# Optimization experiments

Measured on AMD Instinct MI355X. Metric: run time of the kernel, lower is better.

Reference implementation:

```python
import jax, jax.numpy as jnp
import numpy as np

N, C, NS = 131072, 128, 16
BN_EPS = 1e-5


def setup_inputs() -> dict:
    key = jax.random.key(0)
    ks = jax.random.split(key, 8)
    p = jax.random.normal(ks[0], (N, 3), dtype=jnp.float32)
    u = jax.random.normal(ks[1], (N, C), dtype=jnp.float32)
    o = jnp.array([N], dtype=jnp.int32)  # batch offset (single cloud)
    idx = jax.random.randint(ks[2], (N, NS), 0, N, dtype=jnp.int32)  # precomputed KNN indices
    s = 1.0 / np.sqrt(C)
    W1 = jax.random.uniform(ks[3], (C, C), jnp.float32, -s, s)
    b1 = jax.random.uniform(ks[4], (C,), jnp.float32, -s, s)
    W2 = jax.random.uniform(ks[5], (C, C), jnp.float32, -s, s)
    b2 = jax.random.uniform(ks[6], (C,), jnp.float32, -s, s)
    gamma = jnp.ones((C,), jnp.float32)
    beta = jnp.zeros((C,), jnp.float32)
    return {"p": p, "u": u, "o": o, "idx": idx, "W1": W1, "b1": b1,
            "W2": W2, "b2": b2, "gamma": gamma, "beta": beta}


def reference(p, u, o, idx, W1, b1, W2, b2, gamma, beta):
    # pre_trans: Linear(d_in, d_in)
    u_pre = u @ W1 + b1                                  # [N, C]
    # queryandgroup (use_xyz=False): gather neighbor features by KNN idx
    u_n = u_pre[idx]                                     # [N, NS, C] irregular gather
    # local Laplacian: ReLU(neighbor - center), mean over neighborhood
    lap = jnp.maximum(u_n - u_pre[:, None, :], 0.0).mean(axis=1)  # [N, C]
    # varphi: Linear -> BatchNorm1d (training stats) -> ReLU
    h = lap @ W2 + b2                                    # [N, C]
    mean = h.mean(axis=0)
    var = ((h - mean) ** 2).mean(axis=0)  # biased var, as BN normalization uses
    h = (h - mean) * jax.lax.rsqrt(var + BN_EPS) * gamma + beta
    u_tt = jnp.maximum(h, 0.0)
    return (p, u_tt, o)
```

## Files before the change

kernel.cpp:

```cpp
#include <hip/hip_runtime.h>

#define N_PTS 131072
#define C_DIM 128
#define NS_K  16
#define BN_EPS 1e-5f

typedef unsigned short ushort_t;
typedef unsigned short u16x8 __attribute__((ext_vector_type(8)));
typedef __bf16 bf16x8 __attribute__((ext_vector_type(8)));
typedef float f32x4 __attribute__((ext_vector_type(4)));

__device__ __forceinline__ ushort_t f2b(float f) {
    unsigned int u = __float_as_uint(f);
    u += 0x7FFFu + ((u >> 16) & 1u);
    return (ushort_t)(u >> 16);
}
__device__ __forceinline__ float b2f(ushort_t h) {
    return __uint_as_float((unsigned int)h << 16);
}

__global__ __launch_bounds__(256) void prep_w_kernel(
    const float* __restrict__ W1, const float* __restrict__ W2,
    ushort_t* __restrict__ wT1, ushort_t* __restrict__ wT2)
{
    const int t = blockIdx.x * 256 + threadIdx.x;
    const int n = t & 127;
    const int k = t >> 7;
    wT1[n * 128 + k] = f2b(W1[k * 128 + n]);
    wT2[n * 128 + k] = f2b(W2[k * 128 + n]);
}

template <bool A_BF16, bool STATS>
__global__ __launch_bounds__(256) void gemm_mfma_kernel(
    const void* __restrict__ Aptr, const ushort_t* __restrict__ wT,
    const float* __restrict__ bias, ushort_t* __restrict__ out,
    float* __restrict__ gsum, float* __restrict__ gsq)
{
    __shared__ __align__(16) ushort_t a_sh[128 * 136];
    __shared__ __align__(16) ushort_t w_sh[128 * 136];
    __shared__ float s_sum[128];
    __shared__ float s_sq[128];

    const int tid  = threadIdx.x;
    const int lane = tid & 63;
    const int wv   = tid >> 6;
    const int m16  = lane & 15;
    const int q    = lane >> 4;
    const int base = blockIdx.x * 128;

    if (STATS && tid < 128) { s_sum[tid] = 0.f; s_sq[tid] = 0.f; }

    {
        const int row  = tid >> 1;
        const int half = (tid & 1) * 64;
        ushort_t* as = a_sh + row * 136 + half;
        if (A_BF16) {
            const ushort_t* ag = (const ushort_t*)Aptr + (size_t)(base + row) * 128 + half;
            #pragma unroll
            for (int j = 0; j < 8; j++)
                *(u16x8*)(as + j * 8) = *(const u16x8*)(ag + j * 8);
        } else {
            const float* ag = (const float*)Aptr + (size_t)(base + row) * 128 + half;
            #pragma unroll
            for (int j = 0; j < 8; j++) {
                f32x4 lo = *(const f32x4*)(ag + j * 8);
                f32x4 hi = *(const f32x4*)(ag + j * 8 + 4);
                u16x8 v;
                v[0] = f2b(lo[0]); v[1] = f2b(lo[1]); v[2] = f2b(lo[2]); v[3] = f2b(lo[3]);
                v[4] = f2b(hi[0]); v[5] = f2b(hi[1]); v[6] = f2b(hi[2]); v[7] = f2b(hi[3]);
                *(u16x8*)(as + j * 8) = v;
            }
        }
    }
    {
        const int n    = tid >> 1;
        const int half = (tid & 1) * 64;
        const ushort_t* wg = wT + (size_t)n * 128 + half;
        ushort_t* ws = w_sh + n * 136 + half;
        #pragma unroll
        for (int j = 0; j < 8; j++)
            *(u16x8*)(ws + j * 8) = *(const u16x8*)(wg + j * 8);
    }
    __syncthreads();

    f32x4 acc[2][8];
    #pragma unroll
    for (int i = 0; i < 2; i++)
        #pragma unroll
        for (int c = 0; c < 8; c++) acc[i][c] = (f32x4){0.f, 0.f, 0.f, 0.f};

    const ushort_t* ap0 = a_sh + ((wv * 2 + 0) * 16 + m16) * 136 + q * 8;
    const ushort_t* ap1 = a_sh + ((wv * 2 + 1) * 16 + m16) * 136 + q * 8;
    const ushort_t* wp  = w_sh + m16 * 136 + q * 8;

    #pragma unroll
    for (int k0 = 0; k0 < 128; k0 += 32) {
        bf16x8 a0 = __builtin_bit_cast(bf16x8, *(const u16x8*)(ap0 + k0));
        bf16x8 a1 = __builtin_bit_cast(bf16x8, *(const u16x8*)(ap1 + k0));
        #pragma unroll
        for (int c = 0; c < 8; c++) {
            bf16x8 b = __builtin_bit_cast(bf16x8, *(const u16x8*)(wp + c * (16 * 136) + k0));
            acc[0][c] = __builtin_amdgcn_mfma_f32_16x16x32_bf16(a0, b, acc[0][c], 0, 0, 0);
            acc[1][c] = __builtin_amdgcn_mfma_f32_16x16x32_bf16(a1, b, acc[1][c], 0, 0, 0);
        }
    }

    __syncthreads();

    float psum[8], psq[8];
    #pragma unroll
    for (int c = 0; c < 8; c++) { psum[c] = 0.f; psq[c] = 0.f; }

    #pragma unroll
    for (int c = 0; c < 8; c++) {
        const int col = c * 16 + m16;
        const float bv = bias[col];
        #pragma unroll
        for (int i = 0; i < 2; i++) {
            const int rb = (wv * 2 + i) * 16 + q * 4;
            #pragma unroll
            for (int r = 0; r < 4; r++) {
                const float v = acc[i][c][r] + bv;
                a_sh[(rb + r) * 136 + col] = f2b(v);
                if (STATS) { psum[c] += v; psq[c] += v * v; }
            }
        }
    }
    if (STATS) {
        #pragma unroll
        for (int c = 0; c < 8; c++) {
            atomicAdd(&s_sum[c * 16 + m16], psum[c]);
            atomicAdd(&s_sq[c * 16 + m16],  psq[c]);
        }
    }
    __syncthreads();

    {
        const int r0 = tid >> 4;
        const int c0 = (tid & 15) * 8;
        #pragma unroll
        for (int it = 0; it < 8; it++) {
            const int rl = r0 + it * 16;
            const u16x8 v = *(const u16x8*)(a_sh + rl * 136 + c0);
            *(u16x8*)(out + (size_t)(base + rl) * 128 + c0) = v;
        }
    }
    if (STATS && tid < 128) {
        atomicAdd(&gsum[tid], s_sum[tid]);
        atomicAdd(&gsq[tid],  s_sq[tid]);
    }
}

__global__ __launch_bounds__(256) void laplacian_kernel(
    const ushort_t* __restrict__ table, const int* __restrict__ idx,
    ushort_t* __restrict__ lap)
{
    __shared__ int s_idx[256];
    const int tid = threadIdx.x;
    s_idx[tid] = idx[blockIdx.x * 256 + tid];
    __syncthreads();

    const int p  = tid >> 4;
    const int c8 = (tid & 15) * 8;
    const size_t pt = (size_t)blockIdx.x * 16 + p;

    const u16x8 cv = *(const u16x8*)(table + pt * 128 + c8);
    float ctr[8];
    #pragma unroll
    for (int e = 0; e < 8; e++) ctr[e] = b2f(cv[e]);

    float acc[8];
    #pragma unroll
    for (int e = 0; e < 8; e++) acc[e] = 0.f;

    #pragma unroll
    for (int s = 0; s < NS_K; s++) {
        const int j = s_idx[p * 16 + s];
        const u16x8 nv = *(const u16x8*)(table + (size_t)j * 128 + c8);
        #pragma unroll
        for (int e = 0; e < 8; e++)
            acc[e] += fmaxf(b2f(nv[e]) - ctr[e], 0.f);
    }

    u16x8 o;
    #pragma unroll
    for (int e = 0; e < 8; e++) o[e] = f2b(acc[e] * (1.f / (float)NS_K));
    *(u16x8*)(lap + pt * 128 + c8) = o;
}

__global__ void bn_stats_kernel(const float* __restrict__ gsum,
                                const float* __restrict__ gsq,
                                const float* __restrict__ gamma,
                                const float* __restrict__ beta,
                                float* __restrict__ bnsc, float* __restrict__ bnsh)
{
    const int c = threadIdx.x;
    const float invN = 1.f / (float)N_PTS;
    const float mean = gsum[c] * invN;
    const float var  = gsq[c] * invN - mean * mean;
    const float sc   = rsqrtf(var + BN_EPS) * gamma[c];
    bnsc[c] = sc;
    bnsh[c] = fmaf(-mean, sc, beta[c]);
}

__global__ __launch_bounds__(256) void bn_relu_kernel(
    const ushort_t* __restrict__ h, const float* __restrict__ bnsc,
    const float* __restrict__ bnsh, float* __restrict__ out)
{
    const size_t i = (size_t)blockIdx.x * 256 + threadIdx.x;
    const int c8 = (threadIdx.x * 8) & 127;

    const u16x8 hv = *(const u16x8*)(h + i * 8);
    const f32x4 sc0 = *(const f32x4*)(bnsc + c8);
    const f32x4 sc1 = *(const f32x4*)(bnsc + c8 + 4);
    const f32x4 sh0 = *(const f32x4*)(bnsh + c8);
    const f32x4 sh1 = *(const f32x4*)(bnsh + c8 + 4);

    f32x4 o0, o1;
    #pragma unroll
    for (int e = 0; e < 4; e++) {
        o0[e] = fmaxf(fmaf(b2f(hv[e]),     sc0[e], sh0[e]), 0.f);
        o1[e] = fmaxf(fmaf(b2f(hv[4 + e]), sc1[e], sh1[e]), 0.f);
    }
    float* op = out + (size_t)3 * N_PTS + i * 8;
    *(f32x4*)(op)     = o0;
    *(f32x4*)(op + 4) = o1;
}

__global__ __launch_bounds__(256) void copy_p_kernel(
    const float* __restrict__ p, const int* __restrict__ o,
    float* __restrict__ out)
{
    const size_t i = (size_t)blockIdx.x * 256 + threadIdx.x;
    *(f32x4*)(out + i * 4) = *(const f32x4*)(p + i * 4);
    if (i == 0)
        out[(size_t)3 * N_PTS + (size_t)N_PTS * C_DIM] = (float)o[0];
}

extern "C" void kernel_launch(void* const* d_in, const int* in_sizes, int n_in,
                              void* d_out, int out_size, void* d_ws, size_t ws_size,
                              hipStream_t stream) {
    const float* p     = (const float*)d_in[0];
    const float* u     = (const float*)d_in[1];
    const int*   o     = (const int*)d_in[2];
    const int*   idx   = (const int*)d_in[3];
    const float* W1    = (const float*)d_in[4];
    const float* b1    = (const float*)d_in[5];
    const float* W2    = (const float*)d_in[6];
    const float* b2    = (const float*)d_in[7];
    const float* gamma = (const float*)d_in[8];
    const float* beta  = (const float*)d_in[9];
    float* out = (float*)d_out;

    char* ws = (char*)d_ws;
    const size_t buf_bytes = (size_t)N_PTS * C_DIM * sizeof(ushort_t);
    ushort_t* table = (ushort_t*)ws;
    ushort_t* lap   = (ushort_t*)(ws + buf_bytes);
    ushort_t* h     = (ushort_t*)(ws + 2 * buf_bytes);
    float*    stats = (float*)(ws + 3 * buf_bytes);
    float* gsum = stats;
    float* gsq  = stats + 128;
    float* bnsc = stats + 256;
    float* bnsh = stats + 384;
    ushort_t* wT1 = (ushort_t*)(stats + 512);
    ushort_t* wT2 = wT1 + 128 * 128;

    hipMemsetAsync(stats, 0, 256 * sizeof(float), stream);

    prep_w_kernel<<<64, 256, 0, stream>>>(W1, W2, wT1, wT2);
    gemm_mfma_kernel<false, false><<<N_PTS / 128, 256, 0, stream>>>(
        u, wT1, b1, table, nullptr, nullptr);
    laplacian_kernel<<<N_PTS / 16, 256, 0, stream>>>(table, idx, lap);
    gemm_mfma_kernel<true, true><<<N_PTS / 128, 256, 0, stream>>>(
        lap, wT2, b2, h, gsum, gsq);
    bn_stats_kernel<<<1, 128, 0, stream>>>(gsum, gsq, gamma, beta, bnsc, bnsh);
    bn_relu_kernel<<<(N_PTS * C_DIM / 8) / 256, 256, 0, stream>>>(
        h, bnsc, bnsh, out);
    copy_p_kernel<<<(3 * N_PTS / 4) / 256, 256, 0, stream>>>(p, o, out);
}
```

Measured before the change: 288.3 us.

## Fuse BN stats, BN+ReLU and p-copy into one kernel; read weights from global

Removes the memset by zeroing the stats in the weight-prep kernel. Merges the bn_stats, bn_relu and copy_p kernels into one launch that computes the BN scale and shift per block in shared memory. The GEMM kernels no longer stage the 128x128 weight tile in LDS; B fragments are read straight from global or L2. The GEMMs also get a 3-blocks-per-SM launch bound. This cuts launch count and LDS footprint, but adds repeated global weight reads inside the MFMA loop.

```diff
diff --git a/kernel.cpp b/kernel.cpp
--- a/kernel.cpp
+++ b/kernel.cpp
@@ -21,25 +21,26 @@
 
 __global__ __launch_bounds__(256) void prep_w_kernel(
     const float* __restrict__ W1, const float* __restrict__ W2,
-    ushort_t* __restrict__ wT1, ushort_t* __restrict__ wT2)
+    ushort_t* __restrict__ wT1, ushort_t* __restrict__ wT2,
+    float* __restrict__ stats)
 {
     const int t = blockIdx.x * 256 + threadIdx.x;
     const int n = t & 127;
     const int k = t >> 7;
     wT1[n * 128 + k] = f2b(W1[k * 128 + n]);
     wT2[n * 128 + k] = f2b(W2[k * 128 + n]);
+    if (blockIdx.x == 0) stats[threadIdx.x] = 0.f;
 }
 
 template <bool A_BF16, bool STATS>
-__global__ __launch_bounds__(256) void gemm_mfma_kernel(
+__global__ __launch_bounds__(256, 3) void gemm_mfma_kernel(
     const void* __restrict__ Aptr, const ushort_t* __restrict__ wT,
     const float* __restrict__ bias, ushort_t* __restrict__ out,
     float* __restrict__ gsum, float* __restrict__ gsq)
 {
     __shared__ __align__(16) ushort_t a_sh[128 * 136];
-    __shared__ __align__(16) ushort_t w_sh[128 * 136];
-    __shared__ float s_sum[128];
-    __shared__ float s_sq[128];
+    __shared__ float s_sum[STATS ? 128 : 1];
+    __shared__ float s_sq[STATS ? 128 : 1];
 
     const int tid  = threadIdx.x;
     const int lane = tid & 63;
@@ -72,15 +73,6 @@
             }
         }
     }
-    {
-        const int n    = tid >> 1;
-        const int half = (tid & 1) * 64;
-        const ushort_t* wg = wT + (size_t)n * 128 + half;
-        ushort_t* ws = w_sh + n * 136 + half;
-        #pragma unroll
-        for (int j = 0; j < 8; j++)
-            *(u16x8*)(ws + j * 8) = *(const u16x8*)(wg + j * 8);
-    }
     __syncthreads();
 
     f32x4 acc[2][8];
@@ -91,7 +83,7 @@
 
     const ushort_t* ap0 = a_sh + ((wv * 2 + 0) * 16 + m16) * 136 + q * 8;
     const ushort_t* ap1 = a_sh + ((wv * 2 + 1) * 16 + m16) * 136 + q * 8;
-    const ushort_t* wp  = w_sh + m16 * 136 + q * 8;
+    const ushort_t* wp  = wT + (size_t)m16 * 128 + q * 8;
 
     #pragma unroll
     for (int k0 = 0; k0 < 128; k0 += 32) {
@@ -99,7 +91,8 @@
         bf16x8 a1 = __builtin_bit_cast(bf16x8, *(const u16x8*)(ap1 + k0));
         #pragma unroll
         for (int c = 0; c < 8; c++) {
-            bf16x8 b = __builtin_bit_cast(bf16x8, *(const u16x8*)(wp + c * (16 * 136) + k0));
+            bf16x8 b = __builtin_bit_cast(bf16x8,
+                *(const u16x8*)(wp + c * (16 * 128) + k0));
             acc[0][c] = __builtin_amdgcn_mfma_f32_16x16x32_bf16(a0, b, acc[0][c], 0, 0, 0);
             acc[1][c] = __builtin_amdgcn_mfma_f32_16x16x32_bf16(a1, b, acc[1][c], 0, 0, 0);
         }
@@ -188,53 +181,47 @@
     *(u16x8*)(lap + pt * 128 + c8) = o;
 }
 
-__global__ void bn_stats_kernel(const float* __restrict__ gsum,
-                                const float* __restrict__ gsq,
-                                const float* __restrict__ gamma,
-                                const float* __restrict__ beta,
-                                float* __restrict__ bnsc, float* __restrict__ bnsh)
-{
-    const int c = threadIdx.x;
-    const float invN = 1.f / (float)N_PTS;
-    const float mean = gsum[c] * invN;
-    const float var  = gsq[c] * invN - mean * mean;
-    const float sc   = rsqrtf(var + BN_EPS) * gamma[c];
-    bnsc[c] = sc;
-    bnsh[c] = fmaf(-mean, sc, beta[c]);
-}
-
-__global__ __launch_bounds__(256) void bn_relu_kernel(
-    const ushort_t* __restrict__ h, const float* __restrict__ bnsc,
-    const float* __restrict__ bnsh, float* __restrict__ out)
-{
-    const size_t i = (size_t)blockIdx.x * 256 + threadIdx.x;
-    const int c8 = (threadIdx.x * 8) & 127;
-
-    const u16x8 hv = *(const u16x8*)(h + i * 8);
-    const f32x4 sc0 = *(const f32x4*)(bnsc + c8);
-    const f32x4 sc1 = *(const f32x4*)(bnsc + c8 + 4);
-    const f32x4 sh0 = *(const f32x4*)(bnsh + c8);
-    const f32x4 sh1 = *(const f32x4*)(bnsh + c8 + 4);
-
-    f32x4 o0, o1;
-    #pragma unroll
-    for (int e = 0; e < 4; e++) {
-        o0[e] = fmaxf(fmaf(b2f(hv[e]),     sc0[e], sh0[e]), 0.f);
-        o1[e] = fmaxf(fmaf(b2f(hv[4 + e]), sc1[e], sh1[e]), 0.f);
-    }
-    float* op = out + (size_t)3 * N_PTS + i * 8;
-    *(f32x4*)(op)     = o0;
-    *(f32x4*)(op + 4) = o1;
-}
-
-__global__ __launch_bounds__(256) void copy_p_kernel(
-    const float* __restrict__ p, const int* __restrict__ o,
-    float* __restrict__ out)
-{
-    const size_t i = (size_t)blockIdx.x * 256 + threadIdx.x;
-    *(f32x4*)(out + i * 4) = *(const f32x4*)(p + i * 4);
-    if (i == 0)
-        out[(size_t)3 * N_PTS + (size_t)N_PTS * C_DIM] = (float)o[0];
+__global__ __launch_bounds__(256) void bn_relu_tail_kernel(
+    const ushort_t* __restrict__ h, const float* __restrict__ gsum,
+    const float* __restrict__ gsq, const float* __restrict__ gamma,
+    const float* __restrict__ beta, const float* __restrict__ p,
+    const int* __restrict__ o, float* __restrict__ out)
+{
+    const int bid = blockIdx.x;
+    const int tid = threadIdx.x;
+
+    if (bid < 8192) {
+        __shared__ float s_sc[128];
+        __shared__ float s_sh[128];
+        if (tid < 128) {
+            const float invN = 1.f / (float)N_PTS;
+            const float mean = gsum[tid] * invN;
+            const float var  = gsq[tid] * invN - mean * mean;
+            const float sc   = rsqrtf(var + BN_EPS) * gamma[tid];
+            s_sc[tid] = sc;
+            s_sh[tid] = fmaf(-mean, sc, beta[tid]);
+        }
+        __syncthreads();
+
+        const size_t i = (size_t)bid * 256 + tid;
+        const int c8 = (tid * 8) & 127;
+
+        const u16x8 hv = *(const u16x8*)(h + i * 8);
+        f32x4 o0, o1;
+        #pragma unroll
+        for (int e = 0; e < 4; e++) {
+            o0[e] = fmaxf(fmaf(b2f(hv[e]),     s_sc[c8 + e],     s_sh[c8 + e]),     0.f);
+            o1[e] = fmaxf(fmaf(b2f(hv[4 + e]), s_sc[c8 + 4 + e], s_sh[c8 + 4 + e]), 0.f);
+        }
+        float* op = out + (size_t)3 * N_PTS + i * 8;
+        *(f32x4*)(op)     = o0;
+        *(f32x4*)(op + 4) = o1;
+    } else {
+        const size_t i = (size_t)(bid - 8192) * 256 + tid;
+        *(f32x4*)(out + i * 4) = *(const f32x4*)(p + i * 4);
+        if (bid == 8192 && tid == 0)
+            out[(size_t)3 * N_PTS + (size_t)N_PTS * C_DIM] = (float)o[0];
+    }
 }
 
 extern "C" void kernel_launch(void* const* d_in, const int* in_sizes, int n_in,
@@ -260,21 +247,15 @@
     float*    stats = (float*)(ws + 3 * buf_bytes);
     float* gsum = stats;
     float* gsq  = stats + 128;
-    float* bnsc = stats + 256;
-    float* bnsh = stats + 384;
-    ushort_t* wT1 = (ushort_t*)(stats + 512);
+    ushort_t* wT1 = (ushort_t*)(stats + 256);
     ushort_t* wT2 = wT1 + 128 * 128;
 
-    hipMemsetAsync(stats, 0, 256 * sizeof(float), stream);
-
-    prep_w_kernel<<<64, 256, 0, stream>>>(W1, W2, wT1, wT2);
+    prep_w_kernel<<<64, 256, 0, stream>>>(W1, W2, wT1, wT2, stats);
     gemm_mfma_kernel<false, false><<<N_PTS / 128, 256, 0, stream>>>(
         u, wT1, b1, table, nullptr, nullptr);
     laplacian_kernel<<<N_PTS / 16, 256, 0, stream>>>(table, idx, lap);
     gemm_mfma_kernel<true, true><<<N_PTS / 128, 256, 0, stream>>>(
         lap, wT2, b2, h, gsum, gsq);
-    bn_stats_kernel<<<1, 128, 0, stream>>>(gsum, gsq, gamma, beta, bnsc, bnsh);
-    bn_relu_kernel<<<(N_PTS * C_DIM / 8) / 256, 256, 0, stream>>>(
-        h, bnsc, bnsh, out);
-    copy_p_kernel<<<(3 * N_PTS / 4) / 256, 256, 0, stream>>>(p, o, out);
-}
+    bn_relu_tail_kernel<<<8192 + 384, 256, 0, stream>>>(
+        h, gsum, gsq, gamma, beta, p, o, out);
+}
```

After: 323.5 us. 12.2% more time.

## Fuse all pipeline stages into one cooperative persistent kernel with grid syncs

Applied to the files above, without the earlier changes.

Replaces the seven-kernel launch sequence with one cooperative kernel of 512 blocks. Weight transpose, stats zeroing and the p copy run first, followed by GEMM1, the Laplacian gather, GEMM2 with stats, and BN+ReLU, with grid.sync between stages. The aim is to remove per-launch overhead and inter-kernel gaps. In exchange, each stage runs on a fixed grid of 512 blocks with big LDS use per block, which may cut occupancy and latency hiding during the gather stage. The old launch path is kept as a fallback if the cooperative launch fails.

```diff
diff --git a/kernel.cpp b/kernel.cpp
--- a/kernel.cpp
+++ b/kernel.cpp
@@ -1,9 +1,13 @@
 #include <hip/hip_runtime.h>
+#include <hip/hip_cooperative_groups.h>
+
+namespace cg = cooperative_groups;
 
 #define N_PTS 131072
 #define C_DIM 128
 #define NS_K  16
 #define BN_EPS 1e-5f
+#define GRID_BLOCKS 512
 
 typedef unsigned short ushort_t;
 typedef unsigned short u16x8 __attribute__((ext_vector_type(8)));
@@ -17,6 +21,231 @@
 }
 __device__ __forceinline__ float b2f(ushort_t h) {
     return __uint_as_float((unsigned int)h << 16);
+}
+
+template <bool A_BF16, bool STATS>
+__device__ __forceinline__ void gemm_phase(
+    const void* __restrict__ Aptr, const ushort_t* __restrict__ wT,
+    const float* __restrict__ bias, ushort_t* __restrict__ outp,
+    ushort_t* a_sh, ushort_t* w_sh, float* s_red,
+    float* __restrict__ gsum, float* __restrict__ gsq,
+    const int bid, const int tid)
+{
+    const int lane = tid & 63;
+    const int wv   = tid >> 6;
+    const int m16  = lane & 15;
+    const int q    = lane >> 4;
+
+    {
+        const int n    = tid >> 1;
+        const int half = (tid & 1) * 64;
+        const ushort_t* wg = wT + (size_t)n * 128 + half;
+        ushort_t* wsp = w_sh + n * 136 + half;
+        #pragma unroll
+        for (int j = 0; j < 8; j++)
+            *(u16x8*)(wsp + j * 8) = *(const u16x8*)(wg + j * 8);
+    }
+    if (STATS) s_red[tid] = 0.f;
+
+    float psum[8], psq[8];
+    #pragma unroll
+    for (int c = 0; c < 8; c++) { psum[c] = 0.f; psq[c] = 0.f; }
+
+    for (int st = 0; st < 4; st++) {
+        const int base = (bid * 4 + st) * 64;
+        __syncthreads();
+
+        {
+            const int row = tid >> 2;
+            const int qtr = (tid & 3) * 32;
+            ushort_t* as = a_sh + row * 136 + qtr;
+            if (A_BF16) {
+                const ushort_t* ag = (const ushort_t*)Aptr + (size_t)(base + row) * 128 + qtr;
+                #pragma unroll
+                for (int j = 0; j < 4; j++)
+                    *(u16x8*)(as + j * 8) = *(const u16x8*)(ag + j * 8);
+            } else {
+                const float* ag = (const float*)Aptr + (size_t)(base + row) * 128 + qtr;
+                #pragma unroll
+                for (int j = 0; j < 4; j++) {
+                    f32x4 lo = *(const f32x4*)(ag + j * 8);
+                    f32x4 hi = *(const f32x4*)(ag + j * 8 + 4);
+                    u16x8 v;
+                    v[0] = f2b(lo[0]); v[1] = f2b(lo[1]); v[2] = f2b(lo[2]); v[3] = f2b(lo[3]);
+                    v[4] = f2b(hi[0]); v[5] = f2b(hi[1]); v[6] = f2b(hi[2]); v[7] = f2b(hi[3]);
+                    *(u16x8*)(as + j * 8) = v;
+                }
+            }
+        }
+        __syncthreads();
+
+        f32x4 acc[8];
+        #pragma unroll
+        for (int c = 0; c < 8; c++) acc[c] = (f32x4){0.f, 0.f, 0.f, 0.f};
+
+        const ushort_t* ap = a_sh + (wv * 16 + m16) * 136 + q * 8;
+        const ushort_t* wp = w_sh + m16 * 136 + q * 8;
+
+        #pragma unroll
+        for (int k0 = 0; k0 < 128; k0 += 32) {
+            bf16x8 a = __builtin_bit_cast(bf16x8, *(const u16x8*)(ap + k0));
+            #pragma unroll
+            for (int c = 0; c < 8; c++) {
+                bf16x8 b = __builtin_bit_cast(bf16x8, *(const u16x8*)(wp + c * (16 * 136) + k0));
+                acc[c] = __builtin_amdgcn_mfma_f32_16x16x32_bf16(a, b, acc[c], 0, 0, 0);
+            }
+        }
+        __syncthreads();
+
+        #pragma unroll
+        for (int c = 0; c < 8; c++) {
+            const int col = c * 16 + m16;
+            const float bv = bias[col];
+            const int rb = wv * 16 + q * 4;
+            #pragma unroll
+            for (int r = 0; r < 4; r++) {
+                const float v = acc[c][r] + bv;
+                a_sh[(rb + r) * 136 + col] = f2b(v);
+                if (STATS) { psum[c] += v; psq[c] += v * v; }
+            }
+        }
+        __syncthreads();
+
+        {
+            const int r0 = tid >> 4;
+            const int c0 = (tid & 15) * 8;
+            #pragma unroll
+            for (int it = 0; it < 4; it++) {
+                const int rl = r0 + it * 16;
+                const u16x8 v = *(const u16x8*)(a_sh + rl * 136 + c0);
+                *(u16x8*)(outp + (size_t)(base + rl) * 128 + c0) = v;
+            }
+        }
+    }
+
+    if (STATS) {
+        #pragma unroll
+        for (int c = 0; c < 8; c++) {
+            atomicAdd(&s_red[c * 16 + m16], psum[c]);
+            atomicAdd(&s_red[128 + c * 16 + m16], psq[c]);
+        }
+        __syncthreads();
+        if (tid < 128) {
+            atomicAdd(&gsum[tid], s_red[tid]);
+            atomicAdd(&gsq[tid],  s_red[128 + tid]);
+        }
+    }
+}
+
+__global__ __launch_bounds__(256) void mega_kernel(
+    const float* __restrict__ p, const float* __restrict__ u,
+    const int* __restrict__ o, const int* __restrict__ idx,
+    const float* __restrict__ W1, const float* __restrict__ b1,
+    const float* __restrict__ W2, const float* __restrict__ b2,
+    const float* __restrict__ gamma, const float* __restrict__ beta,
+    float* __restrict__ out, ushort_t* __restrict__ table,
+    ushort_t* __restrict__ lap, ushort_t* __restrict__ h,
+    float* __restrict__ gsum, float* __restrict__ gsq,
+    ushort_t* __restrict__ wT1, ushort_t* __restrict__ wT2)
+{
+    cg::grid_group grid = cg::this_grid();
+
+    __shared__ __align__(16) ushort_t a_sh[64 * 136];
+    __shared__ __align__(16) ushort_t w_sh[128 * 136];
+    __shared__ float s_red[256];
+
+    const int bid = blockIdx.x;
+    const int tid = threadIdx.x;
+    const int t   = bid * 256 + tid;
+
+    if (t < 16384) {
+        const int n = t & 127;
+        const int k = t >> 7;
+        wT1[n * 128 + k] = f2b(W1[k * 128 + n]);
+        wT2[n * 128 + k] = f2b(W2[k * 128 + n]);
+    }
+    if (t < 128) gsum[t] = 0.f;
+    else if (t < 256) gsq[t - 128] = 0.f;
+    if (t < 3 * N_PTS / 4)
+        *(f32x4*)(out + (size_t)t * 4) = *(const f32x4*)(p + (size_t)t * 4);
+    if (t == 0)
+        out[(size_t)3 * N_PTS + (size_t)N_PTS * C_DIM] = (float)o[0];
+
+    __threadfence();
+    grid.sync();
+
+    gemm_phase<false, false>(u, wT1, b1, table, a_sh, w_sh, s_red,
+                             nullptr, nullptr, bid, tid);
+    __threadfence();
+    grid.sync();
+
+    {
+        int* s_idx = (int*)a_sh;
+        const int pp = tid >> 4;
+        const int c8 = (tid & 15) * 8;
+        for (int it = 0; it < 16; it++) {
+            const int ib = bid * 16 + it;
+            __syncthreads();
+            s_idx[tid] = idx[(size_t)ib * 256 + tid];
+            __syncthreads();
+
+            const size_t pt = (size_t)ib * 16 + pp;
+            const u16x8 cv = *(const u16x8*)(table + pt * 128 + c8);
+            float ctr[8], acc[8];
+            #pragma unroll
+            for (int e = 0; e < 8; e++) { ctr[e] = b2f(cv[e]); acc[e] = 0.f; }
+
+            #pragma unroll
+            for (int s = 0; s < NS_K; s++) {
+                const int j = s_idx[pp * 16 + s];
+                const u16x8 nv = *(const u16x8*)(table + (size_t)j * 128 + c8);
+                #pragma unroll
+                for (int e = 0; e < 8; e++)
+                    acc[e] += fmaxf(b2f(nv[e]) - ctr[e], 0.f);
+            }
+            u16x8 ov;
+            #pragma unroll
+            for (int e = 0; e < 8; e++) ov[e] = f2b(acc[e] * (1.f / (float)NS_K));
+            *(u16x8*)(lap + pt * 128 + c8) = ov;
+        }
+    }
+    __threadfence();
+    grid.sync();
+
+    gemm_phase<true, true>(lap, wT2, b2, h, a_sh, w_sh, s_red,
+                           gsum, gsq, bid, tid);
+    __threadfence();
+    grid.sync();
+
+    {
+        float* s_sc  = (float*)a_sh;
+        float* s_sh2 = s_sc + 128;
+        __syncthreads();
+        if (tid < 128) {
+            const float invN = 1.f / (float)N_PTS;
+            const float mean = gsum[tid] * invN;
+            const float var  = gsq[tid] * invN - mean * mean;
+            const float sc   = rsqrtf(var + BN_EPS) * gamma[tid];
+            s_sc[tid]  = sc;
+            s_sh2[tid] = fmaf(-mean, sc, beta[tid]);
+        }
+        __syncthreads();
+
+        const int c8 = (tid * 8) & 127;
+        for (int it = 0; it < 16; it++) {
+            const size_t i = ((size_t)bid * 16 + it) * 256 + tid;
+            const u16x8 hv = *(const u16x8*)(h + i * 8);
+            f32x4 o0, o1;
+            #pragma unroll
+            for (int e = 0; e < 4; e++) {
+                o0[e] = fmaxf(fmaf(b2f(hv[e]),     s_sc[c8 + e],     s_sh2[c8 + e]),     0.f);
+                o1[e] = fmaxf(fmaf(b2f(hv[4 + e]), s_sc[c8 + 4 + e], s_sh2[c8 + 4 + e]), 0.f);
+            }
+            float* op = out + (size_t)3 * N_PTS + i * 8;
+            *(f32x4*)(op)     = o0;
+            *(f32x4*)(op + 4) = o1;
+        }
+    }
 }
 
 __global__ __launch_bounds__(256) void prep_w_kernel(
@@ -265,16 +494,27 @@
     ushort_t* wT1 = (ushort_t*)(stats + 512);
     ushort_t* wT2 = wT1 + 128 * 128;
 
-    hipMemsetAsync(stats, 0, 256 * sizeof(float), stream);
-
-    prep_w_kernel<<<64, 256, 0, stream>>>(W1, W2, wT1, wT2);
-    gemm_mfma_kernel<false, false><<<N_PTS / 128, 256, 0, stream>>>(
-        u, wT1, b1, table, nullptr, nullptr);
-    laplacian_kernel<<<N_PTS / 16, 256, 0, stream>>>(table, idx, lap);
-    gemm_mfma_kernel<true, true><<<N_PTS / 128, 256, 0, stream>>>(
-        lap, wT2, b2, h, gsum, gsq);
-    bn_stats_kernel<<<1, 128, 0, stream>>>(gsum, gsq, gamma, beta, bnsc, bnsh);
-    bn_relu_kernel<<<(N_PTS * C_DIM / 8) / 256, 256, 0, stream>>>(
-        h, bnsc, bnsh, out);
-    copy_p_kernel<<<(3 * N_PTS / 4) / 256, 256, 0, stream>>>(p, o, out);
-}
+    void* kargs[] = { (void*)&p, (void*)&u, (void*)&o, (void*)&idx,
+                      (void*)&W1, (void*)&b1, (void*)&W2, (void*)&b2,
+                      (void*)&gamma, (void*)&beta, (void*)&out,
+                      (void*)&table, (void*)&lap, (void*)&h,
+                      (void*)&gsum, (void*)&gsq, (void*)&wT1, (void*)&wT2 };
+
+    hipError_t err = hipLaunchCooperativeKernel(
+        (const void*)mega_kernel, dim3(GRID_BLOCKS), dim3(256), kargs, 0, stream);
+
+    if (err != hipSuccess) {
+        (void)hipGetLastError();
+        hipMemsetAsync(stats, 0, 256 * sizeof(float), stream);
+        prep_w_kernel<<<64, 256, 0, stream>>>(W1, W2, wT1, wT2);
+        gemm_mfma_kernel<false, false><<<N_PTS / 128, 256, 0, stream>>>(
+            u, wT1, b1, table, nullptr, nullptr);
+        laplacian_kernel<<<N_PTS / 16, 256, 0, stream>>>(table, idx, lap);
+        gemm_mfma_kernel<true, true><<<N_PTS / 128, 256, 0, stream>>>(
+            lap, wT2, b2, h, gsum, gsq);
+        bn_stats_kernel<<<1, 128, 0, stream>>>(gsum, gsq, gamma, beta, bnsc, bnsh);
+        bn_relu_kernel<<<(N_PTS * C_DIM / 8) / 256, 256, 0, stream>>>(
+            h, bnsc, bnsh, out);
+        copy_p_kernel<<<(3 * N_PTS / 4) / 256, 256, 0, stream>>>(p, o, out);
+    }
+}
```

Measured after the change: 681.7 us. 136% more time.
